# Kernel optimization log

Measured on AMD Instinct MI355X. Metric: run time of the kernel, lower is better.

The kernel has to match this reference:

```python
import jax, jax.numpy as jnp
import numpy as np

N = 100000
E = 1000000
IN_C, HID, OUT_C = 128, 128, 40
DROPOUT_P = 0.5
BN_EPS = 1e-5


def setup_inputs() -> dict:
    key = jax.random.key(0)
    ks = jax.random.split(key, 10)
    x = jax.random.normal(ks[0], (N, IN_C), dtype=jnp.float32)
    edge_index = jax.random.randint(ks[1], (2, E), 0, N, dtype=jnp.int32)

    def glorot(k, fan_in, fan_out):
        lim = np.sqrt(6.0 / (fan_in + fan_out)).astype(np.float32)
        return jax.random.uniform(k, (fan_in, fan_out), jnp.float32, -lim, lim)

    return {
        "x": x,
        "edge_index": edge_index,
        "W1": glorot(ks[2], IN_C, HID), "b1": jnp.zeros((HID,), jnp.float32),
        "g1": jnp.ones((HID,), jnp.float32), "be1": jnp.zeros((HID,), jnp.float32),
        "W2": glorot(ks[3], HID, HID), "b2": jnp.zeros((HID,), jnp.float32),
        "g2": jnp.ones((HID,), jnp.float32), "be2": jnp.zeros((HID,), jnp.float32),
        "W3": glorot(ks[4], HID, OUT_C), "b3": jnp.zeros((OUT_C,), jnp.float32),
    }


def _deg_inv_sqrt(dst):
    # degree from destination nodes, +1 for the added self loop (PyG gcn_norm)
    deg = jax.ops.segment_sum(jnp.ones((E,), jnp.float32), dst, num_segments=N) + 1.0
    return jax.lax.rsqrt(deg)


def _gcn_conv(h, W, b, src, dst, dinv):
    # h: [N, Cin] -> [N, Cout]; y = D^-1/2 (A + I) D^-1/2 (h W) + b
    hw = h @ W
    norm = dinv[src] * dinv[dst]                      # [E]
    msg = hw[src] * norm[:, None]                     # [E, Cout] gather (memory-bound)
    agg = jax.ops.segment_sum(msg, dst, num_segments=N)
    agg = agg + hw * (dinv * dinv)[:, None]           # self-loop contribution
    return agg + b


def _batchnorm(h, gamma, beta):
    mu = jnp.mean(h, axis=0)
    var = jnp.mean(jnp.square(h - mu), axis=0)        # biased, training mode
    return (h - mu) * jax.lax.rsqrt(var + BN_EPS) * gamma + beta


def _dropout(h, key):
    keep = jax.random.bernoulli(key, 1.0 - DROPOUT_P, h.shape)
    return jnp.where(keep, h / (1.0 - DROPOUT_P), 0.0)


def reference(x, edge_index, W1, b1, g1, be1, W2, b2, g2, be2, W3, b3):
    src, dst = edge_index[0], edge_index[1]
    dinv = _deg_inv_sqrt(dst)
    dk = jax.random.split(jax.random.key(42), 2)

    h = _gcn_conv(x, W1, b1, src, dst, dinv)
    h = _dropout(jax.nn.relu(_batchnorm(h, g1, be1)), dk[0])

    h = _gcn_conv(h, W2, b2, src, dst, dinv)
    h = _dropout(jax.nn.relu(_batchnorm(h, g2, be2)), dk[1])

    h = _gcn_conv(h, W3, b3, src, dst, dinv)
    return jax.nn.log_softmax(h, axis=1)
```

## Files before the change

kernel.cpp:

```cpp
#include <hip/hip_runtime.h>
#include <math.h>

typedef __attribute__((ext_vector_type(8))) short bf16x8;
typedef __attribute__((ext_vector_type(4))) float f32x4;

__device__ __forceinline__ float bfbits2f(unsigned short b){
  return __uint_as_float(((unsigned)b) << 16);
}
__device__ __forceinline__ unsigned short f2bfbits(float f){
  unsigned u = __float_as_uint(f);
  unsigned r = u + 0x7fffu + ((u >> 16) & 1u);
  return (unsigned short)(r >> 16);
}

__host__ __device__ __forceinline__ unsigned rotl32(unsigned v, int d){
  return (v << d) | (v >> (32 - d));
}
__host__ __device__ __forceinline__ void tf2x32(unsigned k0, unsigned k1,
                                                unsigned c0, unsigned c1,
                                                unsigned &o0, unsigned &o1)
{
  unsigned ks2 = k0 ^ k1 ^ 0x1BD11BDAu;
  unsigned x0 = c0 + k0, x1 = c1 + k1;
#define TFR(r) x0 += x1; x1 = rotl32(x1, r); x1 ^= x0;
  TFR(13) TFR(15) TFR(26) TFR(6)
  x0 += k1;  x1 += ks2 + 1u;
  TFR(17) TFR(29) TFR(16) TFR(24)
  x0 += ks2; x1 += k0 + 2u;
  TFR(13) TFR(15) TFR(26) TFR(6)
  x0 += k0;  x1 += k1 + 3u;
  TFR(17) TFR(29) TFR(16) TFR(24)
  x0 += k1;  x1 += ks2 + 4u;
  TFR(13) TFR(15) TFR(26) TFR(6)
  x0 += ks2; x1 += k0 + 5u;
#undef TFR
  o0 = x0; o1 = x1;
}

__device__ __forceinline__ void gen_mask(unsigned* __restrict__ mask,
                                         unsigned mk0, unsigned mk1,
                                         int g, int total, int M)
{
  for (int wi = g; wi < M; wi += total){
    unsigned bits = 0u;
    #pragma unroll 4
    for (int j = 0; j < 32; j++){
      unsigned w0, w1;
      tf2x32(mk0, mk1, 0u, (unsigned)wi * 32u + (unsigned)j, w0, w1);
      bits |= (((w0 ^ w1) >> 31) << j);
    }
    mask[wi] = bits;
  }
}

__global__ __launch_bounds__(256) void k_countpos(const int* __restrict__ dst,
                                                  int* __restrict__ cnt,
                                                  int* __restrict__ pos, int E)
{
  int g = blockIdx.x * 256 + threadIdx.x;
  int base = g * 4;
  if (base + 3 < E){
    int4 d = ((const int4*)dst)[g];
    int4 p;
    p.x = atomicAdd(&cnt[d.x], 1);
    p.y = atomicAdd(&cnt[d.y], 1);
    p.z = atomicAdd(&cnt[d.z], 1);
    p.w = atomicAdd(&cnt[d.w], 1);
    ((int4*)pos)[g] = p;
  } else {
    for (int j = 0; j < 4; j++){
      int e = base + j;
      if (e < E) pos[e] = atomicAdd(&cnt[dst[e]], 1);
    }
  }
}

__global__ __launch_bounds__(256) void k_blocksum(const int* __restrict__ cnt,
                                                  int* __restrict__ bsum, int N)
{
  __shared__ int sh[256];
  int t = threadIdx.x;
  int base = blockIdx.x * 1024 + t * 4;
  int s = 0;
  #pragma unroll
  for (int j = 0; j < 4; j++){ int i = base + j; if (i < N) s += cnt[i]; }
  sh[t] = s; __syncthreads();
  for (int off = 128; off; off >>= 1){
    if (t < off) sh[t] += sh[t + off];
    __syncthreads();
  }
  if (t == 0) bsum[blockIdx.x] = sh[0];
}

__global__ __launch_bounds__(256) void k_scansums(const int* __restrict__ bsum,
                                                  int* __restrict__ boff,
                                                  int* __restrict__ rowstart,
                                                  int NB, int N)
{
  __shared__ int sh[256];
  int t = threadIdx.x;
  int v = (t < NB) ? bsum[t] : 0;
  sh[t] = v; __syncthreads();
  for (int off = 1; off < 256; off <<= 1){
    int x = sh[t];
    int y = (t >= off) ? sh[t - off] : 0;
    __syncthreads();
    sh[t] = x + y;
    __syncthreads();
  }
  if (t < NB) boff[t] = sh[t] - v;
  if (t == NB - 1) rowstart[N] = sh[t];
}

__global__ __launch_bounds__(256) void k_scanfinal(const int* __restrict__ cnt,
                                                   const int* __restrict__ boff,
                                                   int* __restrict__ rowstart,
                                                   float* __restrict__ dinv, int N)
{
  __shared__ int sh[256];
  int t = threadIdx.x;
  int base = blockIdx.x * 1024 + t * 4;
  int c0 = 0, c1 = 0, c2 = 0, c3 = 0;
  if (base + 0 < N) c0 = cnt[base + 0];
  if (base + 1 < N) c1 = cnt[base + 1];
  if (base + 2 < N) c2 = cnt[base + 2];
  if (base + 3 < N) c3 = cnt[base + 3];
  int s = c0 + c1 + c2 + c3;
  sh[t] = s; __syncthreads();
  for (int off = 1; off < 256; off <<= 1){
    int x = sh[t];
    int y = (t >= off) ? sh[t - off] : 0;
    __syncthreads();
    sh[t] = x + y;
    __syncthreads();
  }
  int excl = sh[t] - s + boff[blockIdx.x];
  if (base + 0 < N){ rowstart[base+0] = excl;          dinv[base+0] = rsqrtf((float)c0 + 1.f); }
  if (base + 1 < N){ rowstart[base+1] = excl+c0;       dinv[base+1] = rsqrtf((float)c1 + 1.f); }
  if (base + 2 < N){ rowstart[base+2] = excl+c0+c1;    dinv[base+2] = rsqrtf((float)c2 + 1.f); }
  if (base + 3 < N){ rowstart[base+3] = excl+c0+c1+c2; dinv[base+3] = rsqrtf((float)c3 + 1.f); }
}

__global__ __launch_bounds__(256) void k_fill(const int* __restrict__ src,
                                              const int* __restrict__ dst,
                                              const int* __restrict__ pos,
                                              const int* __restrict__ rowstart,
                                              int* __restrict__ csr, int E)
{
  int g = blockIdx.x * 256 + threadIdx.x;
  int base = g * 4;
  if (base + 3 < E){
    int4 d = ((const int4*)dst)[g];
    int4 p = ((const int4*)pos)[g];
    int4 s = ((const int4*)src)[g];
    int r0 = rowstart[d.x], r1 = rowstart[d.y], r2 = rowstart[d.z], r3 = rowstart[d.w];
    csr[r0 + p.x] = s.x;
    csr[r1 + p.y] = s.y;
    csr[r2 + p.z] = s.z;
    csr[r3 + p.w] = s.w;
  } else {
    for (int j = 0; j < 4; j++){
      int e = base + j;
      if (e < E) csr[rowstart[dst[e]] + pos[e]] = src[e];
    }
  }
}

__global__ __launch_bounds__(256) void k_wt(const float* __restrict__ W1,
                                            const float* __restrict__ W2,
                                            const float* __restrict__ W3,
                                            unsigned short* __restrict__ WT1,
                                            unsigned short* __restrict__ WT2,
                                            unsigned short* __restrict__ WT3)
{
  const float* W; unsigned short* WT; int Cout, Cpad;
  if (blockIdx.x == 0){ W = W1; WT = WT1; Cout = 128; Cpad = 128; }
  else if (blockIdx.x == 1){ W = W2; WT = WT2; Cout = 128; Cpad = 128; }
  else { W = W3; WT = WT3; Cout = 40; Cpad = 48; }
  int tot = Cpad * 128;
  for (int i = threadIdx.x; i < tot; i += 256){
    int n = i >> 7, k = i & 127;
    float v = (n < Cout) ? W[k * Cout + n] : 0.f;
    WT[i] = f2bfbits(v);
  }
}

template<int NT, int MODE>
__global__ __launch_bounds__(256) void k_gemm_mfma(const void* __restrict__ Ap,
                                                   const unsigned short* __restrict__ WT,
                                                   const float* __restrict__ dinv,
                                                   const float* __restrict__ stats,
                                                   const float* __restrict__ g,
                                                   const float* __restrict__ be,
                                                   const unsigned* __restrict__ mask,
                                                   float invN,
                                                   unsigned short* __restrict__ outb,
                                                   int N, int Cout)
{
  __shared__ uint4 Wl4[NT * 16 * 16];
  __shared__ uint4 Al4[64 * 16];
  __shared__ float bnS[128], bnB[128];
  const int t = threadIdx.x;
  const int w = t >> 6, l = t & 63;
  const long rb0 = (long)blockIdx.x * 64;
  const int wrow0 = w * 16;

  uint4 rawU[4];
  float4 rawF[4][2];
  unsigned mword[4];
  int rr[4], cc[4];
  bool inr[4];
  #pragma unroll
  for (int i = 0; i < 4; i++){
    int idx = i * 64 + l;
    int r = idx >> 4, c = idx & 15;
    long grow = rb0 + wrow0 + r;
    rr[i] = r; cc[i] = c; inr[i] = (grow < N);
    if (inr[i]){
      if (MODE == 0){
        const float* ap = (const float*)Ap + grow * 128 + c * 8;
        rawF[i][0] = *(const float4*)ap;
        rawF[i][1] = *(const float4*)(ap + 4);
      } else {
        rawU[i] = *(const uint4*)((const unsigned short*)Ap + grow * 128 + c * 8);
        mword[i] = mask[((unsigned)grow << 2) + (c >> 2)];
      }
    }
  }

  {
    const uint4* s4 = (const uint4*)WT;
    const int tot = NT * 16 * 16;
    for (int i = t; i < tot; i += 256){
      int n = i >> 4, c = i & 15;
      Wl4[n * 16 + (c ^ (n & 15))] = s4[i];
    }
  }
  if (MODE == 2 && t < 128){
    float ss = 0.f, qq = 0.f;
    #pragma unroll
    for (int i = 0; i < 16; i++){
      ss += stats[i * 256 + t];
      qq += stats[i * 256 + 128 + t];
    }
    float mean = ss * invN;
    float var = fmaxf(qq * invN - mean * mean, 0.f);
    float rstd = rsqrtf(var + 1e-5f);
    float sc = g[t] * rstd;
    bnS[t] = sc;
    bnB[t] = be[t] - mean * sc;
  }
  __syncthreads();

  #pragma unroll
  for (int i = 0; i < 4; i++){
    uint4 chunk = make_uint4(0u, 0u, 0u, 0u);
    if (inr[i]){
      if (MODE == 0){
        chunk.x = (unsigned)f2bfbits(rawF[i][0].x) | ((unsigned)f2bfbits(rawF[i][0].y) << 16);
        chunk.y = (unsigned)f2bfbits(rawF[i][0].z) | ((unsigned)f2bfbits(rawF[i][0].w) << 16);
        chunk.z = (unsigned)f2bfbits(rawF[i][1].x) | ((unsigned)f2bfbits(rawF[i][1].y) << 16);
        chunk.w = (unsigned)f2bfbits(rawF[i][1].z) | ((unsigned)f2bfbits(rawF[i][1].w) << 16);
      } else {
        unsigned mb = mword[i] >> ((cc[i] & 3) * 8);
        const unsigned* rw = &rawU[i].x;
        unsigned* cw = &chunk.x;
        #pragma unroll
        for (int h = 0; h < 4; h++){
          int ch = cc[i] * 8 + 2 * h;
          float f0 = bfbits2f((unsigned short)(rw[h] & 0xffffu));
          float f1 = bfbits2f((unsigned short)(rw[h] >> 16));
          f0 = fmaxf(fmaf(f0, bnS[ch],     bnB[ch]),     0.f);
          f1 = fmaxf(fmaf(f1, bnS[ch + 1], bnB[ch + 1]), 0.f);
          f0 = ((mb >> (2 * h))     & 1u) ? 0.f : f0 * 2.f;
          f1 = ((mb >> (2 * h + 1)) & 1u) ? 0.f : f1 * 2.f;
          cw[h] = (unsigned)f2bfbits(f0) | ((unsigned)f2bfbits(f1) << 16);
        }
      }
    }
    Al4[(wrow0 + rr[i]) * 16 + (cc[i] ^ rr[i])] = chunk;
  }

  const int lm = l & 15, q = l >> 4;

  f32x4 acc[NT];
  #pragma unroll
  for (int nt = 0; nt < NT; nt++){
    acc[nt][0] = 0.f; acc[nt][1] = 0.f; acc[nt][2] = 0.f; acc[nt][3] = 0.f;
  }

  #pragma unroll
  for (int kt = 0; kt < 4; kt++){
    const int x = kt * 4 + q;
    bf16x8 a = *(const bf16x8*)&Al4[(wrow0 + lm) * 16 + (x ^ lm)];
    #pragma unroll
    for (int nt = 0; nt < NT; nt++){
      int brow = nt * 16 + lm;
      bf16x8 b = *(const bf16x8*)&Wl4[brow * 16 + (x ^ (brow & 15))];
      acc[nt] = __builtin_amdgcn_mfma_f32_16x16x32_bf16(a, b, acc[nt], 0, 0, 0);
    }
  }

  #pragma unroll
  for (int r = 0; r < 4; r++){
    long row = rb0 + wrow0 + q * 4 + r;
    if (row < N){
      float dv = dinv[row];
      #pragma unroll
      for (int nt = 0; nt < NT; nt++){
        int col = nt * 16 + lm;
        if (col < Cout)
          outb[row * Cout + col] = f2bfbits(acc[nt][r] * dv);
      }
    }
  }
}

#define ACC8(U) do{ uint4 _u = (U); \
  a0 += bfbits2f((unsigned short)(_u.x & 0xffffu)); \
  a1 += bfbits2f((unsigned short)(_u.x >> 16)); \
  a2 += bfbits2f((unsigned short)(_u.y & 0xffffu)); \
  a3 += bfbits2f((unsigned short)(_u.y >> 16)); \
  a4 += bfbits2f((unsigned short)(_u.z & 0xffffu)); \
  a5 += bfbits2f((unsigned short)(_u.z >> 16)); \
  a6 += bfbits2f((unsigned short)(_u.w & 0xffffu)); \
  a7 += bfbits2f((unsigned short)(_u.w >> 16)); }while(0)

__global__ __launch_bounds__(256) void k_agg128s(const unsigned short* __restrict__ hw,
                                                 const int* __restrict__ rs,
                                                 const int* __restrict__ csr,
                                                 const float* __restrict__ dinv,
                                                 unsigned short* __restrict__ outb,
                                                 float* __restrict__ stats,
                                                 unsigned* __restrict__ mask,
                                                 unsigned mk0, unsigned mk1, int M,
                                                 int N)
{
  const int l = threadIdx.x;
  const int ns = l >> 4;
  const int sl = l & 15;
  const int ty = threadIdx.y;
  const int grp = ty * 4 + ns;
  const uint4* h16 = (const uint4*)hw;
  const int base = blockIdx.x * 32;

  gen_mask(mask, mk0, mk1, blockIdx.x * 256 + ty * 64 + l, gridDim.x * 256, M);

  float s0=0.f,s1=0.f,s2=0.f,s3=0.f,s4=0.f,s5=0.f,s6=0.f,s7=0.f;
  float q0=0.f,q1=0.f,q2=0.f,q3=0.f,q4=0.f,q5=0.f,q6=0.f,q7=0.f;

  #pragma unroll 1
  for (int it = 0; it < 2; it++){
    int v = base + it * 16 + grp;
    if (v < N){
      float a0=0.f,a1=0.f,a2=0.f,a3=0.f,a4=0.f,a5=0.f,a6=0.f,a7=0.f;
      ACC8(h16[(size_t)v * 16 + sl]);
      int e0 = rs[v], e1 = rs[v + 1];
      int i = e0;
      for (; i + 4 <= e1; i += 4){
        int sa = csr[i], sb = csr[i+1], sc = csr[i+2], sd = csr[i+3];
        uint4 m0 = h16[(size_t)sa * 16 + sl];
        uint4 m1 = h16[(size_t)sb * 16 + sl];
        uint4 m2 = h16[(size_t)sc * 16 + sl];
        uint4 m3 = h16[(size_t)sd * 16 + sl];
        ACC8(m0); ACC8(m1); ACC8(m2); ACC8(m3);
      }
      for (; i < e1; i++){
        ACC8(h16[(size_t)csr[i] * 16 + sl]);
      }
      float dv = dinv[v];
      a0*=dv; a1*=dv; a2*=dv; a3*=dv; a4*=dv; a5*=dv; a6*=dv; a7*=dv;
      uint4 o;
      o.x = (unsigned)f2bfbits(a0) | ((unsigned)f2bfbits(a1) << 16);
      o.y = (unsigned)f2bfbits(a2) | ((unsigned)f2bfbits(a3) << 16);
      o.z = (unsigned)f2bfbits(a4) | ((unsigned)f2bfbits(a5) << 16);
      o.w = (unsigned)f2bfbits(a6) | ((unsigned)f2bfbits(a7) << 16);
      ((uint4*)outb)[(size_t)v * 16 + sl] = o;
      s0+=a0; q0=fmaf(a0,a0,q0);  s1+=a1; q1=fmaf(a1,a1,q1);
      s2+=a2; q2=fmaf(a2,a2,q2);  s3+=a3; q3=fmaf(a3,a3,q3);
      s4+=a4; q4=fmaf(a4,a4,q4);  s5+=a5; q5=fmaf(a5,a5,q5);
      s6+=a6; q6=fmaf(a6,a6,q6);  s7+=a7; q7=fmaf(a7,a7,q7);
    }
  }

  __shared__ float shS[16][128], shQ[16][128];
  *(float4*)&shS[grp][sl * 8]     = make_float4(s0, s1, s2, s3);
  *(float4*)&shS[grp][sl * 8 + 4] = make_float4(s4, s5, s6, s7);
  *(float4*)&shQ[grp][sl * 8]     = make_float4(q0, q1, q2, q3);
  *(float4*)&shQ[grp][sl * 8 + 4] = make_float4(q4, q5, q6, q7);
  __syncthreads();
  int t = ty * 64 + threadIdx.x;
  if (t < 128){
    float ss = 0.f, qq = 0.f;
    #pragma unroll
    for (int g2 = 0; g2 < 16; g2++){ ss += shS[g2][t]; qq += shQ[g2][t]; }
    float* dstat = stats + (blockIdx.x & 15) * 256;
    atomicAdd(&dstat[t], ss);
    atomicAdd(&dstat[128 + t], qq);
  }
}

__global__ __launch_bounds__(256) void k_agg40lsm(const unsigned short* __restrict__ hw,
                                                  const int* __restrict__ rs,
                                                  const int* __restrict__ csr,
                                                  const float* __restrict__ dinv,
                                                  const float* __restrict__ b3,
                                                  float* __restrict__ out, int N)
{
  const int l = threadIdx.x;
  const int ns = l >> 4, sl = l & 15;
  const int v = blockIdx.x * 16 + threadIdx.y * 4 + ns;
  const bool act = (v < N) && (sl < 10);
  const uint2* h2 = (const uint2*)hw;
  float a0 = 0.f, a1 = 0.f, a2 = 0.f, a3 = 0.f, dv = 1.f;
  if (act){
    dv = dinv[v];
    uint2 u = h2[(size_t)v * 10 + sl];
    a0 = bfbits2f((unsigned short)(u.x & 0xffffu));
    a1 = bfbits2f((unsigned short)(u.x >> 16));
    a2 = bfbits2f((unsigned short)(u.y & 0xffffu));
    a3 = bfbits2f((unsigned short)(u.y >> 16));
    int e0 = rs[v], e1 = rs[v + 1];
    int i = e0;
#define ACCU2(U) do{ uint2 _u = (U); \
    a0 += bfbits2f((unsigned short)(_u.x & 0xffffu)); \
    a1 += bfbits2f((unsigned short)(_u.x >> 16)); \
    a2 += bfbits2f((unsigned short)(_u.y & 0xffffu)); \
    a3 += bfbits2f((unsigned short)(_u.y >> 16)); }while(0)
    for (; i + 4 <= e1; i += 4){
      int sa = csr[i], sb = csr[i+1], sc = csr[i+2], sd = csr[i+3];
      uint2 m0 = h2[(size_t)sa * 10 + sl];
      uint2 m1 = h2[(size_t)sb * 10 + sl];
      uint2 m2 = h2[(size_t)sc * 10 + sl];
      uint2 m3 = h2[(size_t)sd * 10 + sl];
      ACCU2(m0); ACCU2(m1); ACCU2(m2); ACCU2(m3);
    }
    for (; i < e1; i++){
      ACCU2(h2[(size_t)csr[i] * 10 + sl]);
    }
#undef ACCU2
  }
  float x0 = act ? fmaf(a0, dv, b3[sl * 4 + 0]) : -INFINITY;
  float x1 = act ? fmaf(a1, dv, b3[sl * 4 + 1]) : -INFINITY;
  float x2 = act ? fmaf(a2, dv, b3[sl * 4 + 2]) : -INFINITY;
  float x3 = act ? fmaf(a3, dv, b3[sl * 4 + 3]) : -INFINITY;
  float m = fmaxf(fmaxf(x0, x1), fmaxf(x2, x3));
  #pragma unroll
  for (int off = 8; off; off >>= 1) m = fmaxf(m, __shfl_xor(m, off, 16));
  float e = act ? (expf(x0 - m) + expf(x1 - m) + expf(x2 - m) + expf(x3 - m)) : 0.f;
  #pragma unroll
  for (int off = 8; off; off >>= 1) e += __shfl_xor(e, off, 16);
  float lse = m + logf(e);
  if (act){
    float4 o;
    o.x = x0 - lse; o.y = x1 - lse; o.z = x2 - lse; o.w = x3 - lse;
    *reinterpret_cast<float4*>(out + (size_t)v * 40 + sl * 4) = o;
  }
}

extern "C" void kernel_launch(void* const* d_in, const int* in_sizes, int n_in,
                              void* d_out, int out_size, void* d_ws, size_t ws_size,
                              hipStream_t stream)
{
  const float* x  = (const float*)d_in[0];
  const int* ei   = (const int*)d_in[1];
  const float* W1 = (const float*)d_in[2];
  const float* g1 = (const float*)d_in[4];
  const float* be1= (const float*)d_in[5];
  const float* W2 = (const float*)d_in[6];
  const float* g2 = (const float*)d_in[8];
  const float* be2= (const float*)d_in[9];
  const float* W3 = (const float*)d_in[10];
  const float* b3 = (const float*)d_in[11];
  float* out = (float*)d_out;

  const int N = in_sizes[0] / 128;
  const int E = in_sizes[1] / 2;
  const int* srcv = ei;
  const int* dstv = ei + E;

  char* ws = (char*)d_ws;
  size_t off = 0;
  auto take = [&](size_t bytes) -> void* {
    void* p = ws + off;
    off = (off + bytes + 255) & ~(size_t)255;
    return p;
  };
  int*   cnt      = (int*)  take((size_t)N * 4);
  int*   pos      = (int*)  take((size_t)E * 4);
  int*   rowstart = (int*)  take((size_t)(N + 1) * 4);
  int*   csr      = (int*)  take((size_t)E * 4);
  float* dinv     = (float*)take((size_t)N * 4);
  int*   bsum     = (int*)  take(256 * 4);
  int*   boff     = (int*)  take(256 * 4);
  float* stats1   = (float*)take(2 * 16 * 256 * 4);
  float* stats2   = stats1 + 16 * 256;
  unsigned* mask1 = (unsigned*)take((size_t)N * 4 * 4);
  unsigned* mask2 = (unsigned*)take((size_t)N * 4 * 4);
  unsigned short* WT1 = (unsigned short*)take(128 * 128 * 2);
  unsigned short* WT2 = (unsigned short*)take(128 * 128 * 2);
  unsigned short* WT3 = (unsigned short*)take(48 * 128 * 2);
  unsigned short* bufX = (unsigned short*)take((size_t)N * 128 * 2);
  unsigned short* bufY = (unsigned short*)take((size_t)N * 128 * 2);
  (void)ws_size; (void)n_in; (void)out_size;

  unsigned l1k0, l1k1, l2k0, l2k1;
  tf2x32(0u, 42u, 0u, 0u, l1k0, l1k1);
  tf2x32(0u, 42u, 0u, 1u, l2k0, l2k1);

  const float invN = 1.0f / (float)N;
  const int M = N * 4;
  const int NB = (N + 1023) / 1024;
  dim3 wblk(64, 4);
  dim3 wgrid16((N + 15) / 16);
  dim3 wgrid32((N + 31) / 32);
  const int ggrid = (N + 63) / 64;
  const int egrid = (E + 1023) / 1024;

  hipMemsetAsync(cnt, 0, (size_t)N * 4, stream);
  hipMemsetAsync(stats1, 0, 2 * 16 * 256 * 4, stream);
  k_countpos<<<egrid, 256, 0, stream>>>(dstv, cnt, pos, E);
  k_blocksum<<<NB, 256, 0, stream>>>(cnt, bsum, N);
  k_scansums<<<1, 256, 0, stream>>>(bsum, boff, rowstart, NB, N);
  k_scanfinal<<<NB, 256, 0, stream>>>(cnt, boff, rowstart, dinv, N);
  k_fill<<<egrid, 256, 0, stream>>>(srcv, dstv, pos, rowstart, csr, E);
  k_wt<<<3, 256, 0, stream>>>(W1, W2, W3, WT1, WT2, WT3);

  k_gemm_mfma<8, 0><<<ggrid, 256, 0, stream>>>(x, WT1, dinv,
      nullptr, nullptr, nullptr, nullptr, invN, bufX, N, 128);
  k_agg128s<<<wgrid32, wblk, 0, stream>>>(bufX, rowstart, csr, dinv, bufY, stats1,
      mask1, l1k0, l1k1, M, N);

  k_gemm_mfma<8, 2><<<ggrid, 256, 0, stream>>>(bufY, WT2, dinv,
      stats1, g1, be1, mask1, invN, bufX, N, 128);
  k_agg128s<<<wgrid32, wblk, 0, stream>>>(bufX, rowstart, csr, dinv, bufY, stats2,
      mask2, l2k0, l2k1, M, N);

  k_gemm_mfma<3, 2><<<ggrid, 256, 0, stream>>>(bufY, WT3, dinv,
      stats2, g2, be2, mask2, invN, bufX, N, 40);
  k_agg40lsm<<<wgrid16, wblk, 0, stream>>>(bufX, rowstart, csr, dinv, b3, out, N);
}
```

Before: 401.0 us.

## Interleave dropout mask hashing with gather loads in aggregation kernel

Replaces the up-front dropout mask generation loop in the aggregation kernel with per-thread 16-bit mask chunks whose Threefry hashing is interleaved four bits at a time into the edge gather loop, so ALU work can hide memory latency. Each thread now writes one 16-bit word, and any remaining hashing happens after the loop. Separately, the CSR count and fill kernels process two edges per thread instead of four, doubling their grid. The aliasing of 16-bit writes onto the 32-bit mask buffer relies on little-endian bit order matching the consumer's indexing.

```diff
diff --git a/kernel.cpp b/kernel.cpp
--- a/kernel.cpp
+++ b/kernel.cpp
@@ -37,41 +37,20 @@
   o0 = x0; o1 = x1;
 }
 
-__device__ __forceinline__ void gen_mask(unsigned* __restrict__ mask,
-                                         unsigned mk0, unsigned mk1,
-                                         int g, int total, int M)
-{
-  for (int wi = g; wi < M; wi += total){
-    unsigned bits = 0u;
-    #pragma unroll 4
-    for (int j = 0; j < 32; j++){
-      unsigned w0, w1;
-      tf2x32(mk0, mk1, 0u, (unsigned)wi * 32u + (unsigned)j, w0, w1);
-      bits |= (((w0 ^ w1) >> 31) << j);
-    }
-    mask[wi] = bits;
-  }
-}
-
 __global__ __launch_bounds__(256) void k_countpos(const int* __restrict__ dst,
                                                   int* __restrict__ cnt,
                                                   int* __restrict__ pos, int E)
 {
   int g = blockIdx.x * 256 + threadIdx.x;
-  int base = g * 4;
-  if (base + 3 < E){
-    int4 d = ((const int4*)dst)[g];
-    int4 p;
+  int base = g * 2;
+  if (base + 1 < E){
+    int2 d = ((const int2*)dst)[g];
+    int2 p;
     p.x = atomicAdd(&cnt[d.x], 1);
     p.y = atomicAdd(&cnt[d.y], 1);
-    p.z = atomicAdd(&cnt[d.z], 1);
-    p.w = atomicAdd(&cnt[d.w], 1);
-    ((int4*)pos)[g] = p;
-  } else {
-    for (int j = 0; j < 4; j++){
-      int e = base + j;
-      if (e < E) pos[e] = atomicAdd(&cnt[dst[e]], 1);
-    }
+    ((int2*)pos)[g] = p;
+  } else if (base < E){
+    pos[base] = atomicAdd(&cnt[dst[base]], 1);
   }
 }
 
@@ -148,21 +127,16 @@
                                               int* __restrict__ csr, int E)
 {
   int g = blockIdx.x * 256 + threadIdx.x;
-  int base = g * 4;
-  if (base + 3 < E){
-    int4 d = ((const int4*)dst)[g];
-    int4 p = ((const int4*)pos)[g];
-    int4 s = ((const int4*)src)[g];
-    int r0 = rowstart[d.x], r1 = rowstart[d.y], r2 = rowstart[d.z], r3 = rowstart[d.w];
+  int base = g * 2;
+  if (base + 1 < E){
+    int2 d = ((const int2*)dst)[g];
+    int2 p = ((const int2*)pos)[g];
+    int2 s = ((const int2*)src)[g];
+    int r0 = rowstart[d.x], r1 = rowstart[d.y];
     csr[r0 + p.x] = s.x;
     csr[r1 + p.y] = s.y;
-    csr[r2 + p.z] = s.z;
-    csr[r3 + p.w] = s.w;
-  } else {
-    for (int j = 0; j < 4; j++){
-      int e = base + j;
-      if (e < E) csr[rowstart[dst[e]] + pos[e]] = src[e];
-    }
+  } else if (base < E){
+    csr[rowstart[dst[base]] + pos[base]] = src[base];
   }
 }
 
@@ -326,14 +300,22 @@
   a6 += bfbits2f((unsigned short)(_u.w & 0xffffu)); \
   a7 += bfbits2f((unsigned short)(_u.w >> 16)); }while(0)
 
+#define HASH4 do{ if (jm < 16){ \
+  _Pragma("unroll") \
+  for (int jj = 0; jj < 4; jj++){ \
+    unsigned h0, h1; \
+    tf2x32(mk0, mk1, 0u, cbase + (unsigned)(jm + jj), h0, h1); \
+    mbits |= (((h0 ^ h1) >> 31) << (jm + jj)); \
+  } jm += 4; } }while(0)
+
 __global__ __launch_bounds__(256) void k_agg128s(const unsigned short* __restrict__ hw,
                                                  const int* __restrict__ rs,
                                                  const int* __restrict__ csr,
                                                  const float* __restrict__ dinv,
                                                  unsigned short* __restrict__ outb,
                                                  float* __restrict__ stats,
-                                                 unsigned* __restrict__ mask,
-                                                 unsigned mk0, unsigned mk1, int M,
+                                                 unsigned short* __restrict__ mask16,
+                                                 unsigned mk0, unsigned mk1, int N8,
                                                  int N)
 {
   const int l = threadIdx.x;
@@ -344,7 +326,10 @@
   const uint4* h16 = (const uint4*)hw;
   const int base = blockIdx.x * 32;
 
-  gen_mask(mask, mk0, mk1, blockIdx.x * 256 + ty * 64 + l, gridDim.x * 256, M);
+  const int si = blockIdx.x * 256 + ty * 64 + l;
+  const unsigned cbase = (unsigned)si * 16u;
+  unsigned mbits = 0u;
+  int jm = 0;
 
   float s0=0.f,s1=0.f,s2=0.f,s3=0.f,s4=0.f,s5=0.f,s6=0.f,s7=0.f;
   float q0=0.f,q1=0.f,q2=0.f,q3=0.f,q4=0.f,q5=0.f,q6=0.f,q7=0.f;
@@ -363,10 +348,13 @@
         uint4 m1 = h16[(size_t)sb * 16 + sl];
         uint4 m2 = h16[(size_t)sc * 16 + sl];
         uint4 m3 = h16[(size_t)sd * 16 + sl];
+        HASH4;
         ACC8(m0); ACC8(m1); ACC8(m2); ACC8(m3);
       }
       for (; i < e1; i++){
-        ACC8(h16[(size_t)csr[i] * 16 + sl]);
+        uint4 m0 = h16[(size_t)csr[i] * 16 + sl];
+        HASH4;
+        ACC8(m0);
       }
       float dv = dinv[v];
       a0*=dv; a1*=dv; a2*=dv; a3*=dv; a4*=dv; a5*=dv; a6*=dv; a7*=dv;
@@ -382,6 +370,9 @@
       s6+=a6; q6=fmaf(a6,a6,q6);  s7+=a7; q7=fmaf(a7,a7,q7);
     }
   }
+
+  while (jm < 16){ HASH4; }
+  if (si < N8) mask16[si] = (unsigned short)mbits;
 
   __shared__ float shS[16][128], shQ[16][128];
   *(float4*)&shS[grp][sl * 8]     = make_float4(s0, s1, s2, s3);
@@ -509,32 +500,32 @@
   tf2x32(0u, 42u, 0u, 1u, l2k0, l2k1);
 
   const float invN = 1.0f / (float)N;
-  const int M = N * 4;
+  const int N8 = N * 8;
   const int NB = (N + 1023) / 1024;
   dim3 wblk(64, 4);
   dim3 wgrid16((N + 15) / 16);
   dim3 wgrid32((N + 31) / 32);
   const int ggrid = (N + 63) / 64;
-  const int egrid = (E + 1023) / 1024;
+  const int egrid2 = (E + 511) / 512;
 
   hipMemsetAsync(cnt, 0, (size_t)N * 4, stream);
   hipMemsetAsync(stats1, 0, 2 * 16 * 256 * 4, stream);
-  k_countpos<<<egrid, 256, 0, stream>>>(dstv, cnt, pos, E);
+  k_countpos<<<egrid2, 256, 0, stream>>>(dstv, cnt, pos, E);
   k_blocksum<<<NB, 256, 0, stream>>>(cnt, bsum, N);
   k_scansums<<<1, 256, 0, stream>>>(bsum, boff, rowstart, NB, N);
   k_scanfinal<<<NB, 256, 0, stream>>>(cnt, boff, rowstart, dinv, N);
-  k_fill<<<egrid, 256, 0, stream>>>(srcv, dstv, pos, rowstart, csr, E);
+  k_fill<<<egrid2, 256, 0, stream>>>(srcv, dstv, pos, rowstart, csr, E);
   k_wt<<<3, 256, 0, stream>>>(W1, W2, W3, WT1, WT2, WT3);
 
   k_gemm_mfma<8, 0><<<ggrid, 256, 0, stream>>>(x, WT1, dinv,
       nullptr, nullptr, nullptr, nullptr, invN, bufX, N, 128);
   k_agg128s<<<wgrid32, wblk, 0, stream>>>(bufX, rowstart, csr, dinv, bufY, stats1,
-      mask1, l1k0, l1k1, M, N);
+      (unsigned short*)mask1, l1k0, l1k1, N8, N);
 
   k_gemm_mfma<8, 2><<<ggrid, 256, 0, stream>>>(bufY, WT2, dinv,
       stats1, g1, be1, mask1, invN, bufX, N, 128);
   k_agg128s<<<wgrid32, wblk, 0, stream>>>(bufX, rowstart, csr, dinv, bufY, stats2,
-      mask2, l2k0, l2k1, M, N);
+      (unsigned short*)mask2, l2k0, l2k1, N8, N);
 
   k_gemm_mfma<3, 2><<<ggrid, 256, 0, stream>>>(bufY, WT3, dinv,
       stats2, g2, be2, mask2, invN, bufX, N, 40);
```

Measured after the change: 416.0 us. +3.7%, slower.
